# Performance work log

Measured on AMD Instinct MI355X. Metric: run time of the kernel, lower is better.

The kernel has to match this reference:

```python
import jax, jax.numpy as jnp
import numpy as np

H = 64; W = 64; WS = 8; HEADS = 16; DIM = 512
HEAD_DIM = DIM // HEADS
N = WS * WS              # tokens per window
SCALE = HEAD_DIM ** -0.5
EPS = 1e-5


def _rel_pos_index():
    # Same construction as the torch buffer relative_position_index.
    coords = np.stack(np.meshgrid(np.arange(WS), np.arange(WS), indexing='ij'))  # (2, WS, WS)
    cf = coords.reshape(2, -1)                                                   # (2, N)
    rel = (cf[:, :, None] - cf[:, None, :]).transpose(1, 2, 0).copy()            # (N, N, 2)
    rel[:, :, 0] += WS - 1
    rel[:, :, 1] += WS - 1
    rel[:, :, 0] *= 2 * WS - 1
    return jnp.asarray(rel.sum(-1))  # (N, N) int

REL_IDX = _rel_pos_index()


def _layernorm(x, w, b):
    mu = jnp.mean(x, axis=-1, keepdims=True)
    var = jnp.mean(jnp.square(x - mu), axis=-1, keepdims=True)
    return (x - mu) * jax.lax.rsqrt(var + EPS) * w + b


def _window_partition(x):
    # x: (B, H, W, C) -> (nW*B, N, C)
    B, _, _, C = x.shape
    x = x.reshape(B, H // WS, WS, W // WS, WS, C).transpose(0, 1, 3, 2, 4, 5)
    return x.reshape(-1, N, C)


def _window_reverse(win, B):
    C = win.shape[-1]
    x = win.reshape(B, H // WS, W // WS, WS, WS, C).transpose(0, 1, 3, 2, 4, 5)
    return x.reshape(B, H, W, C)


def _qkv(x, w, b):
    # x: (B_, N, C); w: (C, 3C); b: (3C,) -> q,k,v each (B_, heads, N, hd)
    B_, n, C = x.shape
    t = (x @ w + b).reshape(B_, n, 3, HEADS, HEAD_DIM).transpose(2, 0, 3, 1, 4)
    return t[0], t[1], t[2]


def setup_inputs() -> dict:
    key = jax.random.key(0)
    ks = jax.random.split(key, 12)
    B = 16
    s = 0.02
    return {
        'x1': jax.random.normal(ks[0], (B, H * W, DIM), jnp.float32),
        'x2': jax.random.normal(ks[1], (B, H * W, DIM), jnp.float32),
        'norm1_w': jnp.ones((DIM,), jnp.float32),
        'norm1_b': jnp.zeros((DIM,), jnp.float32),
        'norm2_w': jnp.ones((DIM,), jnp.float32),
        'norm2_b': jnp.zeros((DIM,), jnp.float32),
        'qkv1_w': jax.random.normal(ks[2], (DIM, 3 * DIM), jnp.float32) * s,
        'qkv1_b': jnp.zeros((3 * DIM,), jnp.float32),
        'qkv2_w': jax.random.normal(ks[3], (DIM, 3 * DIM), jnp.float32) * s,
        'qkv2_b': jnp.zeros((3 * DIM,), jnp.float32),
        'rpb_table': jax.random.normal(ks[4], ((2 * WS - 1) * (2 * WS - 1), HEADS), jnp.float32) * s,
        'proj_w': jax.random.normal(ks[5], (DIM, DIM), jnp.float32) * s,
        'proj_b': jnp.zeros((DIM,), jnp.float32),
    }


def reference(x1, x2, norm1_w, norm1_b, norm2_w, norm2_b,
              qkv1_w, qkv1_b, qkv2_w, qkv2_b, rpb_table, proj_w, proj_b):
    B, L, C = x1.shape
    shortcut = x1

    # BeforeCrossAttention for each image (shift_size=0 -> no roll)
    w1 = _window_partition(_layernorm(x1, norm1_w, norm1_b).reshape(B, H, W, C))  # rescaled
    w2 = _window_partition(_layernorm(x2, norm2_w, norm2_b).reshape(B, H, W, C))  # rescaler

    q1, k1, v1 = _qkv(w1, qkv1_w, qkv1_b)   # rescaled
    q2, k2, v2 = _qkv(w2, qkv2_w, qkv2_b)   # rescaler
    # same_key_query=False: q from rescaler, k & v from rescaled
    q, k, v = q2 * SCALE, k1, v1

    attn = jnp.einsum('bhnd,bhmd->bhnm', q, k)                       # (nW*B, heads, N, N)
    bias = rpb_table[REL_IDX.reshape(-1)].reshape(N, N, HEADS).transpose(2, 0, 1)
    attn = jax.nn.softmax(attn + bias[None], axis=-1)

    out = jnp.einsum('bhnm,bhmd->bhnd', attn, v)                     # (nW*B, heads, N, hd)
    out = out.transpose(0, 2, 1, 3).reshape(-1, N, C)
    out = out @ proj_w + proj_b

    out = _window_reverse(out, B).reshape(B, L, C)
    return shortcut + out
```

## Files before the change

### kernel.cpp

```cpp
#include <hip/hip_runtime.h>
#include <hip/hip_bf16.h>

typedef __attribute__((ext_vector_type(8))) short short8;
typedef __attribute__((ext_vector_type(4))) float f32x4;

#define SCALE 0.17677669529663687f

__device__ __forceinline__ unsigned short f2bf(float f) {
    union { __hip_bfloat16 b; unsigned short u; } c;
    c.b = __float2bfloat16(f);
    return c.u;
}

__device__ __forceinline__ void gload_lds16(const unsigned short* g, unsigned short* l) {
    __builtin_amdgcn_global_load_lds((const __attribute__((address_space(1))) void*)g,
                                     (__attribute__((address_space(3))) void*)l, 16, 0, 0);
}

__global__ __launch_bounds__(256) void ln_kernel(
    const float* __restrict__ x1, const float* __restrict__ x2,
    const float* __restrict__ n1w, const float* __restrict__ n1b,
    const float* __restrict__ n2w, const float* __restrict__ n2b,
    unsigned short* __restrict__ xn1, unsigned short* __restrict__ xn2)
{
    int lane = threadIdx.x & 63;
    int row  = blockIdx.x * 4 + (threadIdx.x >> 6);
    const float* src; const float* w; const float* b; unsigned short* dst;
    if (row < 65536) {
        src = x1 + (size_t)row * 512; w = n1w; b = n1b; dst = xn1 + (size_t)row * 512;
    } else {
        size_t r = (size_t)(row - 65536);
        src = x2 + r * 512; w = n2w; b = n2b; dst = xn2 + r * 512;
    }
    float4 v0 = *(const float4*)(src + lane * 4);
    float4 v1 = *(const float4*)(src + 256 + lane * 4);
    float s = v0.x + v0.y + v0.z + v0.w + v1.x + v1.y + v1.z + v1.w;
    float q = v0.x*v0.x + v0.y*v0.y + v0.z*v0.z + v0.w*v0.w
            + v1.x*v1.x + v1.y*v1.y + v1.z*v1.z + v1.w*v1.w;
#pragma unroll
    for (int m = 1; m < 64; m <<= 1) { s += __shfl_xor(s, m); q += __shfl_xor(q, m); }
    float mu  = s * (1.0f / 512.0f);
    float var = q * (1.0f / 512.0f) - mu * mu;
    float rs  = rsqrtf(var + 1e-5f);
    float4 w0 = *(const float4*)(w + lane * 4);
    float4 w1 = *(const float4*)(w + 256 + lane * 4);
    float4 b0 = *(const float4*)(b + lane * 4);
    float4 b1 = *(const float4*)(b + 256 + lane * 4);
    ushort4 o0, o1;
    o0.x = f2bf((v0.x - mu) * rs * w0.x + b0.x);
    o0.y = f2bf((v0.y - mu) * rs * w0.y + b0.y);
    o0.z = f2bf((v0.z - mu) * rs * w0.z + b0.z);
    o0.w = f2bf((v0.w - mu) * rs * w0.w + b0.w);
    o1.x = f2bf((v1.x - mu) * rs * w1.x + b1.x);
    o1.y = f2bf((v1.y - mu) * rs * w1.y + b1.y);
    o1.z = f2bf((v1.z - mu) * rs * w1.z + b1.z);
    o1.w = f2bf((v1.w - mu) * rs * w1.w + b1.w);
    *(ushort4*)(dst + lane * 4)       = o0;
    *(ushort4*)(dst + 256 + lane * 4) = o1;
}

__global__ __launch_bounds__(256) void wconv_kernel(
    const float* __restrict__ qkv1_w, const float* __restrict__ qkv2_w,
    const float* __restrict__ proj_w,
    unsigned short* __restrict__ WqT, unsigned short* __restrict__ WkvT,
    unsigned short* __restrict__ WpT)
{
    __shared__ float tile[32][33];
    int t = blockIdx.x;
    const float* src; int ldin, c0, tn, tk; unsigned short* dst;
    if (t < 256)      { src = qkv2_w; ldin = 1536; c0 = 0;   dst = WqT;  tn = t >> 4;        tk = t & 15; }
    else if (t < 768) { int u = t - 256; src = qkv1_w; ldin = 1536; c0 = 512; dst = WkvT; tn = u >> 4; tk = u & 15; }
    else              { int u = t - 768; src = proj_w; ldin = 512;  c0 = 0;   dst = WpT;  tn = u >> 4; tk = u & 15; }
    int lx = threadIdx.x & 31, ly = threadIdx.x >> 5;
#pragma unroll
    for (int i = 0; i < 4; i++)
        tile[ly + i * 8][lx] = src[(size_t)(tk * 32 + ly + i * 8) * ldin + c0 + tn * 32 + lx];
    __syncthreads();
#pragma unroll
    for (int i = 0; i < 4; i++)
        dst[(size_t)(tn * 32 + ly + i * 8) * 512 + tk * 32 + lx] = f2bf(tile[lx][ly + i * 8]);
}

__device__ __forceinline__ void gemm_core(
    const unsigned short* __restrict__ A,
    const unsigned short* __restrict__ W,
    unsigned short* sA, unsigned short* sB,
    f32x4 acc[4][4])
{
    int tid = threadIdx.x, lane = tid & 63;
    int wv = tid >> 6, wr = wv >> 1, wc = wv & 1;
    int lr = lane & 15, lk = lane >> 4;
    for (int k0 = 0; k0 < 512; k0 += 64) {
#pragma unroll
        for (int i = 0; i < 4; i++) {
            int flat = i * 256 + tid;
            int r = flat >> 3, cc = flat & 7;
            gload_lds16(A + (size_t)r * 512 + k0 + cc * 8, sA + flat * 8);
            gload_lds16(W + (size_t)r * 512 + k0 + cc * 8, sB + flat * 8);
        }
        __syncthreads();
#pragma unroll
        for (int ks = 0; ks < 2; ks++) {
            short8 a[4], b[4];
#pragma unroll
            for (int mi = 0; mi < 4; mi++)
                a[mi] = *(const short8*)(sA + (64 * wr + 16 * mi + lr) * 64 + ks * 32 + lk * 8);
#pragma unroll
            for (int ni = 0; ni < 4; ni++)
                b[ni] = *(const short8*)(sB + (64 * wc + 16 * ni + lr) * 64 + ks * 32 + lk * 8);
#pragma unroll
            for (int mi = 0; mi < 4; mi++)
#pragma unroll
                for (int ni = 0; ni < 4; ni++)
                    acc[mi][ni] = __builtin_amdgcn_mfma_f32_16x16x32_bf16(a[mi], b[ni], acc[mi][ni], 0, 0, 0);
        }
        __syncthreads();
    }
}

__global__ __launch_bounds__(256) void qkv_gemm_kernel(
    const unsigned short* __restrict__ XN1, const unsigned short* __restrict__ XN2,
    const unsigned short* __restrict__ WqT, const unsigned short* __restrict__ WkvT,
    const float* __restrict__ qkv1_b, const float* __restrict__ qkv2_b,
    unsigned short* __restrict__ Qb, unsigned short* __restrict__ KVb)
{
    __shared__ unsigned short sA[128 * 64];
    __shared__ unsigned short sB[128 * 64];
    int mb = blockIdx.x, nb = blockIdx.y;
    f32x4 acc[4][4];
#pragma unroll
    for (int mi = 0; mi < 4; mi++)
#pragma unroll
        for (int ni = 0; ni < 4; ni++) { f32x4 z = {0.f, 0.f, 0.f, 0.f}; acc[mi][ni] = z; }
    const unsigned short* Ap; const unsigned short* Wp;
    if (nb < 4) { Ap = XN2 + (size_t)mb * 128 * 512; Wp = WqT  + (size_t)nb * 128 * 512; }
    else        { Ap = XN1 + (size_t)mb * 128 * 512; Wp = WkvT + (size_t)(nb - 4) * 128 * 512; }
    gemm_core(Ap, Wp, sA, sB, acc);
    int lane = threadIdx.x & 63, wv = threadIdx.x >> 6;
    int wr = wv >> 1, wc = wv & 1, lr = lane & 15, lk = lane >> 4;
    if (nb < 4) {
#pragma unroll
        for (int ni = 0; ni < 4; ni++) {
            int col = nb * 128 + 64 * wc + 16 * ni + lr;
            float bias = qkv2_b[col];
#pragma unroll
            for (int mi = 0; mi < 4; mi++)
#pragma unroll
                for (int i = 0; i < 4; i++) {
                    int row = mb * 128 + 64 * wr + 16 * mi + 4 * lk + i;
                    Qb[(size_t)row * 512 + col] = f2bf((acc[mi][ni][i] + bias) * SCALE);
                }
        }
    } else {
#pragma unroll
        for (int ni = 0; ni < 4; ni++) {
            int col = (nb - 4) * 128 + 64 * wc + 16 * ni + lr;
            float bias = qkv1_b[512 + col];
#pragma unroll
            for (int mi = 0; mi < 4; mi++)
#pragma unroll
                for (int i = 0; i < 4; i++) {
                    int row = mb * 128 + 64 * wr + 16 * mi + 4 * lk + i;
                    KVb[(size_t)row * 1024 + col] = f2bf(acc[mi][ni][i] + bias);
                }
        }
    }
}

__global__ __launch_bounds__(256) void attn_kernel(
    const unsigned short* __restrict__ Qb, const unsigned short* __restrict__ KVb,
    const float* __restrict__ rpb, unsigned short* __restrict__ AO)
{
    __shared__ unsigned short sV[4][64 * 32];
    __shared__ unsigned short sP[4][64 * 64];
    int wv = threadIdx.x >> 6, lane = threadIdx.x & 63;
    int lr = lane & 15, lk = lane >> 4;
    int u = blockIdx.x * 4 + wv;
    int win = u >> 4, h = u & 15;
    int b = win >> 6, wi = win & 63;
    int rowbase = b * 4096 + (wi >> 3) * 512 + (wi & 7) * 8;
    unsigned short* myV = sV[wv];
    unsigned short* myP = sP[wv];

#pragma unroll
    for (int i = 0; i < 4; i++) {
        int c = i * 64 + lane;
        int t = c >> 2, cc = c & 3;
        int grow = rowbase + (t >> 3) * 64 + (t & 7);
        *(short8*)(myV + t * 32 + cc * 8) =
            *(const short8*)(KVb + (size_t)grow * 1024 + 512 + h * 32 + cc * 8);
    }
    short8 qf[4], kf[4];
#pragma unroll
    for (int fr = 0; fr < 4; fr++) {
        int t = 16 * fr + lr;
        int grow = rowbase + (t >> 3) * 64 + (t & 7);
        qf[fr] = *(const short8*)(Qb  + (size_t)grow * 512  + h * 32 + lk * 8);
        kf[fr] = *(const short8*)(KVb + (size_t)grow * 1024 + h * 32 + lk * 8);
    }
    f32x4 s[4][4];
#pragma unroll
    for (int fr = 0; fr < 4; fr++)
#pragma unroll
        for (int fc = 0; fc < 4; fc++) { f32x4 z = {0.f, 0.f, 0.f, 0.f}; s[fr][fc] = z; }
#pragma unroll
    for (int fr = 0; fr < 4; fr++)
#pragma unroll
        for (int fc = 0; fc < 4; fc++)
            s[fr][fc] = __builtin_amdgcn_mfma_f32_16x16x32_bf16(qf[fr], kf[fc], s[fr][fc], 0, 0, 0);

    float rinv[4][4];
#pragma unroll
    for (int fr = 0; fr < 4; fr++) {
#pragma unroll
        for (int i = 0; i < 4; i++) {
            int n = 16 * fr + 4 * lk + i;
#pragma unroll
            for (int fc = 0; fc < 4; fc++) {
                int m = 16 * fc + lr;
                int idx = ((n >> 3) - (m >> 3) + 7) * 15 + (n & 7) - (m & 7) + 7;
                s[fr][fc][i] += rpb[idx * 16 + h];
            }
            float v = fmaxf(fmaxf(s[fr][0][i], s[fr][1][i]), fmaxf(s[fr][2][i], s[fr][3][i]));
            v = fmaxf(v, __shfl_xor(v, 1)); v = fmaxf(v, __shfl_xor(v, 2));
            v = fmaxf(v, __shfl_xor(v, 4)); v = fmaxf(v, __shfl_xor(v, 8));
            float sum = 0.f;
#pragma unroll
            for (int fc = 0; fc < 4; fc++) {
                float e = __expf(s[fr][fc][i] - v);
                s[fr][fc][i] = e; sum += e;
            }
            sum += __shfl_xor(sum, 1); sum += __shfl_xor(sum, 2);
            sum += __shfl_xor(sum, 4); sum += __shfl_xor(sum, 8);
            rinv[fr][i] = 1.0f / sum;
#pragma unroll
            for (int fc = 0; fc < 4; fc++) {
                int m = 16 * fc + lr;
                int chunk = (m >> 3) ^ (n & 7);
                myP[n * 64 + chunk * 8 + (m & 7)] = f2bf(s[fr][fc][i]);
            }
        }
    }
    __syncthreads();

    f32x4 o[4][2];
#pragma unroll
    for (int fr = 0; fr < 4; fr++)
#pragma unroll
        for (int nj = 0; nj < 2; nj++) { f32x4 z = {0.f, 0.f, 0.f, 0.f}; o[fr][nj] = z; }
#pragma unroll
    for (int mk = 0; mk < 2; mk++) {
        short8 pa[4];
#pragma unroll
        for (int fr = 0; fr < 4; fr++) {
            int n = 16 * fr + lr;
            int chunk = (4 * mk + lk) ^ (n & 7);
            pa[fr] = *(const short8*)(myP + n * 64 + chunk * 8);
        }
#pragma unroll
        for (int nj = 0; nj < 2; nj++) {
            short8 vb;
#pragma unroll
            for (int j = 0; j < 8; j++)
                vb[j] = (short)myV[(32 * mk + 8 * lk + j) * 32 + 16 * nj + lr];
#pragma unroll
            for (int fr = 0; fr < 4; fr++)
                o[fr][nj] = __builtin_amdgcn_mfma_f32_16x16x32_bf16(pa[fr], vb, o[fr][nj], 0, 0, 0);
        }
    }
#pragma unroll
    for (int fr = 0; fr < 4; fr++)
#pragma unroll
        for (int nj = 0; nj < 2; nj++)
#pragma unroll
            for (int i = 0; i < 4; i++) {
                int t = 16 * fr + 4 * lk + i;
                int grow = rowbase + (t >> 3) * 64 + (t & 7);
                AO[(size_t)grow * 512 + h * 32 + 16 * nj + lr] = f2bf(o[fr][nj][i] * rinv[fr][i]);
            }
}

__global__ __launch_bounds__(256) void proj_gemm_kernel(
    const unsigned short* __restrict__ AO, const unsigned short* __restrict__ WpT,
    const float* __restrict__ proj_b, const float* __restrict__ x1,
    float* __restrict__ out)
{
    __shared__ unsigned short sA[128 * 64];
    __shared__ unsigned short sB[128 * 64];
    int mb = blockIdx.x, nb = blockIdx.y;
    f32x4 acc[4][4];
#pragma unroll
    for (int mi = 0; mi < 4; mi++)
#pragma unroll
        for (int ni = 0; ni < 4; ni++) { f32x4 z = {0.f, 0.f, 0.f, 0.f}; acc[mi][ni] = z; }
    gemm_core(AO + (size_t)mb * 128 * 512, WpT + (size_t)nb * 128 * 512, sA, sB, acc);
    int lane = threadIdx.x & 63, wv = threadIdx.x >> 6;
    int wr = wv >> 1, wc = wv & 1, lr = lane & 15, lk = lane >> 4;
#pragma unroll
    for (int ni = 0; ni < 4; ni++) {
        int col = nb * 128 + 64 * wc + 16 * ni + lr;
        float bias = proj_b[col];
#pragma unroll
        for (int mi = 0; mi < 4; mi++)
#pragma unroll
            for (int i = 0; i < 4; i++) {
                int row = mb * 128 + 64 * wr + 16 * mi + 4 * lk + i;
                out[(size_t)row * 512 + col] = acc[mi][ni][i] + bias + x1[(size_t)row * 512 + col];
            }
    }
}

extern "C" void kernel_launch(void* const* d_in, const int* in_sizes, int n_in,
                              void* d_out, int out_size, void* d_ws, size_t ws_size,
                              hipStream_t stream)
{
    const float* x1     = (const float*)d_in[0];
    const float* x2     = (const float*)d_in[1];
    const float* n1w    = (const float*)d_in[2];
    const float* n1b    = (const float*)d_in[3];
    const float* n2w    = (const float*)d_in[4];
    const float* n2b    = (const float*)d_in[5];
    const float* qkv1_w = (const float*)d_in[6];
    const float* qkv1_b = (const float*)d_in[7];
    const float* qkv2_w = (const float*)d_in[8];
    const float* qkv2_b = (const float*)d_in[9];
    const float* rpb    = (const float*)d_in[10];
    const float* proj_w = (const float*)d_in[11];
    const float* proj_b = (const float*)d_in[12];
    float* out = (float*)d_out;

    char* ws = (char*)d_ws;
    const size_t SZ = 67108864;
    unsigned short* XN1  = (unsigned short*)(ws);
    unsigned short* XN2  = (unsigned short*)(ws + SZ);
    unsigned short* Qb   = (unsigned short*)(ws + 2 * SZ);
    unsigned short* KVb  = (unsigned short*)(ws + 3 * SZ);
    unsigned short* WqT  = (unsigned short*)(ws + 5 * SZ);
    unsigned short* WkvT = WqT + 512 * 512;
    unsigned short* WpT  = WkvT + 1024 * 512;
    unsigned short* AO   = XN2;

    hipLaunchKernelGGL(ln_kernel,        dim3(32768),   dim3(256), 0, stream,
                       x1, x2, n1w, n1b, n2w, n2b, XN1, XN2);
    hipLaunchKernelGGL(wconv_kernel,     dim3(1024),    dim3(256), 0, stream,
                       qkv1_w, qkv2_w, proj_w, WqT, WkvT, WpT);
    hipLaunchKernelGGL(qkv_gemm_kernel,  dim3(512, 12), dim3(256), 0, stream,
                       XN1, XN2, WqT, WkvT, qkv1_b, qkv2_b, Qb, KVb);
    hipLaunchKernelGGL(attn_kernel,      dim3(4096),    dim3(256), 0, stream,
                       Qb, KVb, rpb, AO);
    hipLaunchKernelGGL(proj_gemm_kernel, dim3(512, 4),  dim3(256), 0, stream,
                       AO, WpT, proj_b, x1, out);
}
```

Baseline: 727.4 us.

## Replace GEMMs with 256x256-tile, double-buffered, swizzled-LDS pipelined MFMA kernels

Both the QKV and projection GEMMs now use 256x256 output tiles with 512-thread blocks and 8 waves, each wave computing a 128x64 sub-tile. Global-to-LDS direct loads are double-buffered across half-k-steps and gated by explicit vmcnt waits, so loads overlap the MFMAs. The LDS layout is XOR-swizzled to avoid bank conflicts, s_setprio is raised around the MFMA bursts, and block IDs are remapped for XCD/L2 locality. The larger tile cuts global traffic per FLOP, at the cost of more registers, 128KB of LDS and fewer blocks in flight.

```diff
diff --git a/kernel.cpp b/kernel.cpp
--- a/kernel.cpp
+++ b/kernel.cpp
@@ -81,89 +81,170 @@
         dst[(size_t)(tn * 32 + ly + i * 8) * 512 + tk * 32 + lx] = f2bf(tile[lx][ly + i * 8]);
 }
 
-__device__ __forceinline__ void gemm_core(
-    const unsigned short* __restrict__ A,
-    const unsigned short* __restrict__ W,
-    unsigned short* sA, unsigned short* sB,
-    f32x4 acc[4][4])
-{
-    int tid = threadIdx.x, lane = tid & 63;
-    int wv = tid >> 6, wr = wv >> 1, wc = wv & 1;
+
+__device__ __forceinline__ void stage_unit(
+    unsigned short* lds, const unsigned short* A, const unsigned short* W,
+    int tile, int s, int wv, int sr, int sq, int dst_lane)
+{
+    int buf = (tile & 1) << 15;
+    int k0  = tile * 64 + s * 32;
+#pragma unroll
+    for (int i = 0; i < 2; i++) {
+        int R   = i * 8 + wv;
+        int sub = (R * 2 + s) << 9;
+        gload_lds16(A + (size_t)(R * 16 + sr) * 512 + k0 + sq * 8,
+                    lds + buf + sub + dst_lane);
+        gload_lds16(W + (size_t)(R * 16 + sr) * 512 + k0 + sq * 8,
+                    lds + buf + 16384 + sub + dst_lane);
+    }
+}
+
+template<int VM, bool DOST>
+__device__ __forceinline__ void gphase(
+    unsigned short* lds, const unsigned short* A, const unsigned short* W,
+    f32x4 (&acc)[8][4], int tile, int s, int st_t, int st_s,
+    int wr, int wc, int wv, int rdoff, int sr, int sq, int dst_lane)
+{
+    if constexpr (VM == 8)      asm volatile("s_waitcnt vmcnt(8)" ::: "memory");
+    else if constexpr (VM == 4) asm volatile("s_waitcnt vmcnt(4)" ::: "memory");
+    else                        asm volatile("s_waitcnt vmcnt(0)" ::: "memory");
+    __builtin_amdgcn_s_barrier();
+    __builtin_amdgcn_sched_barrier(0);
+    int buf = (tile & 1) << 15;
+    short8 a[8], b[4];
+#pragma unroll
+    for (int mi = 0; mi < 8; mi++)
+        a[mi] = *(const short8*)(lds + buf + (((wr * 8 + mi) * 2 + s) << 9) + rdoff);
+#pragma unroll
+    for (int ni = 0; ni < 4; ni++)
+        b[ni] = *(const short8*)(lds + buf + 16384 + (((wc * 4 + ni) * 2 + s) << 9) + rdoff);
+    if constexpr (DOST) stage_unit(lds, A, W, st_t, st_s, wv, sr, sq, dst_lane);
+    __builtin_amdgcn_s_setprio(1);
+#pragma unroll
+    for (int mi = 0; mi < 8; mi++)
+#pragma unroll
+        for (int ni = 0; ni < 4; ni++)
+            acc[mi][ni] = __builtin_amdgcn_mfma_f32_16x16x32_bf16(a[mi], b[ni], acc[mi][ni], 0, 0, 0);
+    __builtin_amdgcn_s_setprio(0);
+}
+
+__device__ __forceinline__ void gemm256(
+    unsigned short* lds, const unsigned short* A, const unsigned short* W,
+    f32x4 (&acc)[8][4])
+{
+    int tid = threadIdx.x, lane = tid & 63, wv = tid >> 6;
+    int wr = wv >> 2, wc = wv & 3;
     int lr = lane & 15, lk = lane >> 4;
-    for (int k0 = 0; k0 < 512; k0 += 64) {
-#pragma unroll
-        for (int i = 0; i < 4; i++) {
-            int flat = i * 256 + tid;
-            int r = flat >> 3, cc = flat & 7;
-            gload_lds16(A + (size_t)r * 512 + k0 + cc * 8, sA + flat * 8);
-            gload_lds16(W + (size_t)r * 512 + k0 + cc * 8, sB + flat * 8);
-        }
-        __syncthreads();
-#pragma unroll
-        for (int ks = 0; ks < 2; ks++) {
-            short8 a[4], b[4];
-#pragma unroll
-            for (int mi = 0; mi < 4; mi++)
-                a[mi] = *(const short8*)(sA + (64 * wr + 16 * mi + lr) * 64 + ks * 32 + lk * 8);
-#pragma unroll
-            for (int ni = 0; ni < 4; ni++)
-                b[ni] = *(const short8*)(sB + (64 * wc + 16 * ni + lr) * 64 + ks * 32 + lk * 8);
-#pragma unroll
-            for (int mi = 0; mi < 4; mi++)
-#pragma unroll
-                for (int ni = 0; ni < 4; ni++)
-                    acc[mi][ni] = __builtin_amdgcn_mfma_f32_16x16x32_bf16(a[mi], b[ni], acc[mi][ni], 0, 0, 0);
-        }
-        __syncthreads();
-    }
-}
-
-__global__ __launch_bounds__(256) void qkv_gemm_kernel(
+    int rdoff    = lr * 32 + ((lk ^ ((lr >> 1) & 3)) << 3);
+    int sr       = lane >> 2;
+    int sq       = (lane & 3) ^ ((sr >> 1) & 3);
+    int dst_lane = lane * 8;
+
+    stage_unit(lds, A, W, 0, 0, wv, sr, sq, dst_lane);
+    stage_unit(lds, A, W, 0, 1, wv, sr, sq, dst_lane);
+    stage_unit(lds, A, W, 1, 0, wv, sr, sq, dst_lane);
+    stage_unit(lds, A, W, 1, 1, wv, sr, sq, dst_lane);
+
+    gphase<8,false>(lds, A, W, acc, 0, 0, 0, 0, wr, wc, wv, rdoff, sr, sq, dst_lane);
+    gphase<8,true >(lds, A, W, acc, 0, 1, 2, 0, wr, wc, wv, rdoff, sr, sq, dst_lane);
+    gphase<8,true >(lds, A, W, acc, 1, 0, 2, 1, wr, wc, wv, rdoff, sr, sq, dst_lane);
+    gphase<8,true >(lds, A, W, acc, 1, 1, 3, 0, wr, wc, wv, rdoff, sr, sq, dst_lane);
+    gphase<8,true >(lds, A, W, acc, 2, 0, 3, 1, wr, wc, wv, rdoff, sr, sq, dst_lane);
+    gphase<8,true >(lds, A, W, acc, 2, 1, 4, 0, wr, wc, wv, rdoff, sr, sq, dst_lane);
+    gphase<8,true >(lds, A, W, acc, 3, 0, 4, 1, wr, wc, wv, rdoff, sr, sq, dst_lane);
+    gphase<8,true >(lds, A, W, acc, 3, 1, 5, 0, wr, wc, wv, rdoff, sr, sq, dst_lane);
+    gphase<8,true >(lds, A, W, acc, 4, 0, 5, 1, wr, wc, wv, rdoff, sr, sq, dst_lane);
+    gphase<8,true >(lds, A, W, acc, 4, 1, 6, 0, wr, wc, wv, rdoff, sr, sq, dst_lane);
+    gphase<8,true >(lds, A, W, acc, 5, 0, 6, 1, wr, wc, wv, rdoff, sr, sq, dst_lane);
+    gphase<8,true >(lds, A, W, acc, 5, 1, 7, 0, wr, wc, wv, rdoff, sr, sq, dst_lane);
+    gphase<8,true >(lds, A, W, acc, 6, 0, 7, 1, wr, wc, wv, rdoff, sr, sq, dst_lane);
+    gphase<8,false>(lds, A, W, acc, 6, 1, 0, 0, wr, wc, wv, rdoff, sr, sq, dst_lane);
+    gphase<4,false>(lds, A, W, acc, 7, 0, 0, 0, wr, wc, wv, rdoff, sr, sq, dst_lane);
+    gphase<0,false>(lds, A, W, acc, 7, 1, 0, 0, wr, wc, wv, rdoff, sr, sq, dst_lane);
+}
+
+__global__ __launch_bounds__(512) void qkv_gemm256(
     const unsigned short* __restrict__ XN1, const unsigned short* __restrict__ XN2,
     const unsigned short* __restrict__ WqT, const unsigned short* __restrict__ WkvT,
     const float* __restrict__ qkv1_b, const float* __restrict__ qkv2_b,
     unsigned short* __restrict__ Qb, unsigned short* __restrict__ KVb)
 {
-    __shared__ unsigned short sA[128 * 64];
-    __shared__ unsigned short sB[128 * 64];
-    int mb = blockIdx.x, nb = blockIdx.y;
-    f32x4 acc[4][4];
-#pragma unroll
-    for (int mi = 0; mi < 4; mi++)
-#pragma unroll
-        for (int ni = 0; ni < 4; ni++) { f32x4 z = {0.f, 0.f, 0.f, 0.f}; acc[mi][ni] = z; }
-    const unsigned short* Ap; const unsigned short* Wp;
-    if (nb < 4) { Ap = XN2 + (size_t)mb * 128 * 512; Wp = WqT  + (size_t)nb * 128 * 512; }
-    else        { Ap = XN1 + (size_t)mb * 128 * 512; Wp = WkvT + (size_t)(nb - 4) * 128 * 512; }
-    gemm_core(Ap, Wp, sA, sB, acc);
+    __shared__ unsigned short lds[65536];
+    int bid = blockIdx.x;
+    int wg  = (bid & 7) * 192 + (bid >> 3);
+    int mb  = wg / 6, nb = wg % 6;
+    f32x4 acc[8][4];
+#pragma unroll
+    for (int mi = 0; mi < 8; mi++)
+#pragma unroll
+        for (int ni = 0; ni < 4; ni++) { f32x4 z = {0.f,0.f,0.f,0.f}; acc[mi][ni] = z; }
+    const unsigned short* A; const unsigned short* W;
+    if (nb < 2) { A = XN2 + (size_t)mb * 256 * 512; W = WqT  + (size_t)nb * 256 * 512; }
+    else        { A = XN1 + (size_t)mb * 256 * 512; W = WkvT + (size_t)(nb - 2) * 256 * 512; }
+    gemm256(lds, A, W, acc);
+
     int lane = threadIdx.x & 63, wv = threadIdx.x >> 6;
-    int wr = wv >> 1, wc = wv & 1, lr = lane & 15, lk = lane >> 4;
-    if (nb < 4) {
+    int wr = wv >> 2, wc = wv & 3, lr = lane & 15, lk = lane >> 4;
+    int base_m = mb * 256 + wr * 128;
+    if (nb < 2) {
 #pragma unroll
         for (int ni = 0; ni < 4; ni++) {
-            int col = nb * 128 + 64 * wc + 16 * ni + lr;
+            int col = nb * 256 + wc * 64 + ni * 16 + lr;
             float bias = qkv2_b[col];
 #pragma unroll
-            for (int mi = 0; mi < 4; mi++)
-#pragma unroll
-                for (int i = 0; i < 4; i++) {
-                    int row = mb * 128 + 64 * wr + 16 * mi + 4 * lk + i;
-                    Qb[(size_t)row * 512 + col] = f2bf((acc[mi][ni][i] + bias) * SCALE);
+            for (int mi = 0; mi < 8; mi++)
+#pragma unroll
+                for (int ii = 0; ii < 4; ii++) {
+                    int row = base_m + mi * 16 + lk * 4 + ii;
+                    Qb[(size_t)row * 512 + col] = f2bf((acc[mi][ni][ii] + bias) * SCALE);
                 }
         }
     } else {
 #pragma unroll
         for (int ni = 0; ni < 4; ni++) {
-            int col = (nb - 4) * 128 + 64 * wc + 16 * ni + lr;
+            int col = (nb - 2) * 256 + wc * 64 + ni * 16 + lr;
             float bias = qkv1_b[512 + col];
 #pragma unroll
-            for (int mi = 0; mi < 4; mi++)
-#pragma unroll
-                for (int i = 0; i < 4; i++) {
-                    int row = mb * 128 + 64 * wr + 16 * mi + 4 * lk + i;
-                    KVb[(size_t)row * 1024 + col] = f2bf(acc[mi][ni][i] + bias);
+            for (int mi = 0; mi < 8; mi++)
+#pragma unroll
+                for (int ii = 0; ii < 4; ii++) {
+                    int row = base_m + mi * 16 + lk * 4 + ii;
+                    KVb[(size_t)row * 1024 + col] = f2bf(acc[mi][ni][ii] + bias);
                 }
         }
+    }
+}
+
+__global__ __launch_bounds__(512) void proj_gemm256(
+    const unsigned short* __restrict__ AO, const unsigned short* __restrict__ WpT,
+    const float* __restrict__ proj_b, const float* __restrict__ x1,
+    float* __restrict__ out)
+{
+    __shared__ unsigned short lds[65536];
+    int bid = blockIdx.x;
+    int wg  = (bid & 7) * 64 + (bid >> 3);
+    int mb  = wg >> 1, nb = wg & 1;
+    f32x4 acc[8][4];
+#pragma unroll
+    for (int mi = 0; mi < 8; mi++)
+#pragma unroll
+        for (int ni = 0; ni < 4; ni++) { f32x4 z = {0.f,0.f,0.f,0.f}; acc[mi][ni] = z; }
+    gemm256(lds, AO + (size_t)mb * 256 * 512, WpT + (size_t)nb * 256 * 512, acc);
+
+    int lane = threadIdx.x & 63, wv = threadIdx.x >> 6;
+    int wr = wv >> 2, wc = wv & 3, lr = lane & 15, lk = lane >> 4;
+    int base_m = mb * 256 + wr * 128;
+#pragma unroll
+    for (int ni = 0; ni < 4; ni++) {
+        int col = nb * 256 + wc * 64 + ni * 16 + lr;
+        float bias = proj_b[col];
+#pragma unroll
+        for (int mi = 0; mi < 8; mi++)
+#pragma unroll
+            for (int ii = 0; ii < 4; ii++) {
+                int row = base_m + mi * 16 + lk * 4 + ii;
+                out[(size_t)row * 512 + col] = acc[mi][ni][ii] + bias + x1[(size_t)row * 512 + col];
+            }
     }
 }
 
@@ -202,7 +283,7 @@
 #pragma unroll
     for (int fr = 0; fr < 4; fr++)
 #pragma unroll
-        for (int fc = 0; fc < 4; fc++) { f32x4 z = {0.f, 0.f, 0.f, 0.f}; s[fr][fc] = z; }
+        for (int fc = 0; fc < 4; fc++) { f32x4 z = {0.f,0.f,0.f,0.f}; s[fr][fc] = z; }
 #pragma unroll
     for (int fr = 0; fr < 4; fr++)
 #pragma unroll
@@ -247,7 +328,7 @@
 #pragma unroll
     for (int fr = 0; fr < 4; fr++)
 #pragma unroll
-        for (int nj = 0; nj < 2; nj++) { f32x4 z = {0.f, 0.f, 0.f, 0.f}; o[fr][nj] = z; }
+        for (int nj = 0; nj < 2; nj++) { f32x4 z = {0.f,0.f,0.f,0.f}; o[fr][nj] = z; }
 #pragma unroll
     for (int mk = 0; mk < 2; mk++) {
         short8 pa[4];
@@ -278,36 +359,6 @@
                 int grow = rowbase + (t >> 3) * 64 + (t & 7);
                 AO[(size_t)grow * 512 + h * 32 + 16 * nj + lr] = f2bf(o[fr][nj][i] * rinv[fr][i]);
             }
-}
-
-__global__ __launch_bounds__(256) void proj_gemm_kernel(
-    const unsigned short* __restrict__ AO, const unsigned short* __restrict__ WpT,
-    const float* __restrict__ proj_b, const float* __restrict__ x1,
-    float* __restrict__ out)
-{
-    __shared__ unsigned short sA[128 * 64];
-    __shared__ unsigned short sB[128 * 64];
-    int mb = blockIdx.x, nb = blockIdx.y;
-    f32x4 acc[4][4];
-#pragma unroll
-    for (int mi = 0; mi < 4; mi++)
-#pragma unroll
-        for (int ni = 0; ni < 4; ni++) { f32x4 z = {0.f, 0.f, 0.f, 0.f}; acc[mi][ni] = z; }
-    gemm_core(AO + (size_t)mb * 128 * 512, WpT + (size_t)nb * 128 * 512, sA, sB, acc);
-    int lane = threadIdx.x & 63, wv = threadIdx.x >> 6;
-    int wr = wv >> 1, wc = wv & 1, lr = lane & 15, lk = lane >> 4;
-#pragma unroll
-    for (int ni = 0; ni < 4; ni++) {
-        int col = nb * 128 + 64 * wc + 16 * ni + lr;
-        float bias = proj_b[col];
-#pragma unroll
-        for (int mi = 0; mi < 4; mi++)
-#pragma unroll
-            for (int i = 0; i < 4; i++) {
-                int row = mb * 128 + 64 * wr + 16 * mi + 4 * lk + i;
-                out[(size_t)row * 512 + col] = acc[mi][ni][i] + bias + x1[(size_t)row * 512 + col];
-            }
-    }
 }
 
 extern "C" void kernel_launch(void* const* d_in, const int* in_sizes, int n_in,
@@ -340,14 +391,14 @@
     unsigned short* WpT  = WkvT + 1024 * 512;
     unsigned short* AO   = XN2;
 
-    hipLaunchKernelGGL(ln_kernel,        dim3(32768),   dim3(256), 0, stream,
+    hipLaunchKernelGGL(ln_kernel,     dim3(32768), dim3(256), 0, stream,
                        x1, x2, n1w, n1b, n2w, n2b, XN1, XN2);
-    hipLaunchKernelGGL(wconv_kernel,     dim3(1024),    dim3(256), 0, stream,
+    hipLaunchKernelGGL(wconv_kernel,  dim3(1024),  dim3(256), 0, stream,
                        qkv1_w, qkv2_w, proj_w, WqT, WkvT, WpT);
-    hipLaunchKernelGGL(qkv_gemm_kernel,  dim3(512, 12), dim3(256), 0, stream,
+    hipLaunchKernelGGL(qkv_gemm256,   dim3(1536),  dim3(512), 0, stream,
                        XN1, XN2, WqT, WkvT, qkv1_b, qkv2_b, Qb, KVb);
-    hipLaunchKernelGGL(attn_kernel,      dim3(4096),    dim3(256), 0, stream,
+    hipLaunchKernelGGL(attn_kernel,   dim3(4096),  dim3(256), 0, stream,
                        Qb, KVb, rpb, AO);
-    hipLaunchKernelGGL(proj_gemm_kernel, dim3(512, 4),  dim3(256), 0, stream,
+    hipLaunchKernelGGL(proj_gemm256,  dim3(512),   dim3(512), 0, stream,
                        AO, WpT, proj_b, x1, out);
 }
```

New measurement: 675.9 us. -7.1%, faster.
